# Kernel tuning notes

Hardware: AMD Instinct MI355X
Metric: run time of the kernel (lower is better)

Reference implementation:

```python
import jax, jax.numpy as jnp
import numpy as np

EPS = 1e-8
NUM_HEADS = 4


def setup_inputs() -> dict:
    key = jax.random.key(0)
    ks = jax.random.split(key, 20)
    N, D = 8192, 200      # total nodes, gnn/text dim
    B = 4                  # graphs (text batch)
    E, DEG = 4096, 16      # hyperedges, nodes per hyperedge
    H = 128                # fusion hidden dim
    f = lambda k, s: jax.random.normal(k, s, dtype=jnp.float32) * 0.05
    return {
        "x": jax.random.normal(ks[0], (N, D), dtype=jnp.float32),
        "text": jax.random.normal(ks[1], (B, D), dtype=jnp.float32),
        "W": f(ks[2], (D, D)),
        "b": jnp.zeros((D,), jnp.float32),
        "gate_w": f(ks[3], (D, 1)),
        "gate_b": jnp.zeros((1,), jnp.float32),
        "gnn_w": f(ks[4], (D, H)), "gnn_b": f(ks[5], (H,)),
        "text_w": f(ks[6], (D, H)), "text_b": f(ks[7], (H,)),
        "in_w": f(ks[8], (H, 3 * H)), "in_b": f(ks[9], (3 * H,)),
        "attn_out_w": f(ks[10], (H, H)), "attn_out_b": f(ks[11], (H,)),
        "fgate_w": f(ks[12], (2 * H, H)), "fgate_b": f(ks[13], (H,)),
        "outp_w": f(ks[14], (H, D)), "outp_b": f(ks[15], (D,)),
        "edge_nodes": jax.random.randint(ks[16], (E, DEG), 0, N),
    }


def _forward(x, text, W, b, gate_w, gate_b, gnn_w, gnn_b, text_w, text_b,
             in_w, in_b, attn_out_w, attn_out_b, fgate_w, fgate_b,
             outp_w, outp_b, edge_nodes):
    N, D = x.shape
    E, DEG = edge_nodes.shape
    # --- HypergraphConv: incidence build + normalized Laplacian propagation ---
    out = x @ W                                         # [N, D]
    # H[node, edge] = 1/len(edge); duplicates overwrite (set), as in torch loop
    Hinc = jnp.zeros((N, E), x.dtype).at[edge_nodes, jnp.arange(E)[:, None]].set(1.0 / DEG)
    Dv = Hinc.sum(axis=1)                               # node degree [N]
    De = Hinc.sum(axis=0)                               # edge degree [E]
    dv = 1.0 / jnp.sqrt(Dv + EPS)
    de = 1.0 / (De + EPS)
    Hl = Hinc * dv[:, None]                             # Dv^-1/2 H
    L = (Hl * de[None, :]) @ Hl.T                       # Dv^-1/2 H De^-1 H^T Dv^-1/2
    hyper_out = L @ out                                 # [N, D]
    alpha = jax.nn.sigmoid(x.mean(axis=0, keepdims=True) @ gate_w + gate_b)  # [1,1]
    gnn_feat = alpha * out + (1.0 - alpha) * hyper_out + b
    # --- CrossModalAttentionFusion on per-graph node features (3D path) ---
    B = text.shape[0]
    Nn = N // B
    gnn3 = gnn_feat.reshape(B, Nn, D)
    gp = gnn3 @ gnn_w + gnn_b                           # [B, Nn, H]
    tp = (text @ text_w + text_b)[:, None, :]           # [B, 1, H]
    Hd = gp.shape[-1]
    hd = Hd // NUM_HEADS
    q = gp @ in_w[:, :Hd] + in_b[:Hd]
    k = tp @ in_w[:, Hd:2 * Hd] + in_b[Hd:2 * Hd]
    v = tp @ in_w[:, 2 * Hd:] + in_b[2 * Hd:]
    qh = q.reshape(B, Nn, NUM_HEADS, hd).transpose(0, 2, 1, 3)   # [B,h,Nn,hd]
    kh = k.reshape(B, 1, NUM_HEADS, hd).transpose(0, 2, 1, 3)    # [B,h,1,hd]
    vh = v.reshape(B, 1, NUM_HEADS, hd).transpose(0, 2, 1, 3)
    scores = jnp.einsum("bhqd,bhkd->bhqk", qh, kh) / jnp.sqrt(jnp.float32(hd))
    attn = jax.nn.softmax(scores, axis=-1)              # kv_len=1 -> ones
    att = jnp.einsum("bhqk,bhkd->bhqd", attn, vh)
    att = att.transpose(0, 2, 1, 3).reshape(B, Nn, Hd) @ attn_out_w + attn_out_b
    g = jax.nn.sigmoid(jnp.concatenate([gp, att], axis=-1) @ fgate_w + fgate_b)
    fused = g * gp + (1.0 - g) * att
    return fused @ outp_w + outp_b                      # [B, Nn, D]


def reference(x, text, W, b, gate_w, gate_b, gnn_w, gnn_b, text_w, text_b,
              in_w, in_b, attn_out_w, attn_out_b, fgate_w, fgate_b,
              outp_w, outp_b, edge_nodes):
    return _forward(x, text, W, b, gate_w, gate_b, gnn_w, gnn_b, text_w, text_b,
                    in_w, in_b, attn_out_w, attn_out_b, fgate_w, fgate_b,
                    outp_w, outp_b, edge_nodes)
```

## Files before the change

kernel.cpp:

```cpp
#include <hip/hip_runtime.h>

#define NODES 8192
#define DIM   200
#define NEDGE 4096
#define DEGREE 16
#define HD    128
#define MT    16
#define ECAP  32
#define CPB   512

__device__ __forceinline__ float dv_of(int cnt) {
    return 1.0f / sqrtf((float)cnt * (1.0f / 16.0f) + 1e-8f);
}

__global__ void k_front(const float* __restrict__ W, const float* __restrict__ gnn_w,
                        const float* __restrict__ bias, const float* __restrict__ gnn_b,
                        const float* __restrict__ text, const float* __restrict__ text_w,
                        const float* __restrict__ text_b, const float* __restrict__ in_w,
                        const float* __restrict__ in_b, const float* __restrict__ aow,
                        const float* __restrict__ aob, const float* __restrict__ fgw,
                        const float* __restrict__ fgb, int* __restrict__ cnt,
                        float* __restrict__ Wg, float* __restrict__ bg,
                        float* __restrict__ attO, float* __restrict__ attg) {
    __shared__ float st[DIM];
    __shared__ float part[2][HD];
    __shared__ float vin[HD];
    int b = blockIdx.x, t = threadIdx.x;
    if (b < 32) {
        cnt[b * 256 + t] = 0;
        return;
    }
    if (b < 132) {
        int r = 2 * (b - 32) + (t >> 7);
        int c = t & 127;
        const float* vec = &W[r * DIM];
        float acc = 0.f;
        for (int k = 0; k < DIM; k++) acc += vec[k] * gnn_w[k * HD + c];
        Wg[r * HD + c] = acc;
        return;
    }
    if (b == 132) {
        if (t < HD) {
            float acc = 0.f;
            for (int k = 0; k < DIM; k++) acc += bias[k] * gnn_w[k * HD + t];
            bg[t] = acc + gnn_b[t];
        }
        return;
    }
    int g = b - 133;
    int c = t & 127, h = t >> 7;
    if (t < DIM) st[t] = text[g * DIM + t];
    __syncthreads();
    {
        float acc = 0.f;
        int k0 = h * 100;
        for (int k = k0; k < k0 + 100; k++) acc += st[k] * text_w[k * HD + c];
        part[h][c] = acc;
    }
    __syncthreads();
    if (t < HD) vin[t] = part[0][t] + part[1][t] + text_b[t];
    __syncthreads();
    {
        float acc = 0.f;
        int k0 = h * 64;
        for (int k = k0; k < k0 + 64; k++) acc += vin[k] * in_w[k * 3 * HD + 2 * HD + c];
        part[h][c] = acc;
    }
    __syncthreads();
    if (t < HD) vin[t] = part[0][t] + part[1][t] + in_b[2 * HD + t];
    __syncthreads();
    {
        float acc = 0.f;
        int k0 = h * 64;
        for (int k = k0; k < k0 + 64; k++) acc += vin[k] * aow[k * HD + c];
        part[h][c] = acc;
    }
    __syncthreads();
    if (t < HD) {
        float ao = part[0][t] + part[1][t] + aob[t];
        attO[g * HD + t] = ao;
        vin[t] = ao;
    }
    __syncthreads();
    {
        float acc = 0.f;
        int k0 = h * 64;
        for (int k = k0; k < k0 + 64; k++) acc += vin[k] * fgw[(HD + k) * HD + c];
        part[h][c] = acc;
    }
    __syncthreads();
    if (t < HD) attg[g * HD + t] = part[0][t] + part[1][t] + fgb[t];
}

__global__ void k_xwg(const float* __restrict__ x, const float* __restrict__ Wg,
                      const int* __restrict__ en, float* __restrict__ out2,
                      int* __restrict__ cnt, int* __restrict__ emask,
                      int* __restrict__ elist2, float* __restrict__ cpart) {
    __shared__ float sx[16 * DIM];
    int b = blockIdx.x, t = threadIdx.x;
    int bm = b * 16;
    const float4* x4 = (const float4*)(x + bm * DIM);
    float4* sx4 = (float4*)sx;
    for (int i = t; i < 16 * DIM / 4; i += 256) sx4[i] = x4[i];
    __syncthreads();
    if (t < DIM) {
        float s = 0.f;
#pragma unroll
        for (int r = 0; r < 16; r++) s += sx[r * DIM + t];
        cpart[b * DIM + t] = s;
    }
    int rg = t >> 6;
    int c0 = t & 63;
    float acc[4][2] = {{0.f,0.f},{0.f,0.f},{0.f,0.f},{0.f,0.f}};
    for (int k = 0; k < DIM; k++) {
        float w0 = Wg[k * HD + c0];
        float w1 = Wg[k * HD + c0 + 64];
#pragma unroll
        for (int i = 0; i < 4; i++) {
            float s = sx[(rg * 4 + i) * DIM + k];
            acc[i][0] += s * w0;
            acc[i][1] += s * w1;
        }
    }
#pragma unroll
    for (int i = 0; i < 4; i++) {
        out2[(bm + rg * 4 + i) * HD + c0]      = acc[i][0];
        out2[(bm + rg * 4 + i) * HD + c0 + 64] = acc[i][1];
    }
    if (t < 8) {
        int e = b * 8 + t;
        int idx[DEGREE];
#pragma unroll
        for (int i = 0; i < DEGREE; i++) idx[i] = en[e * DEGREE + i];
        int mask = 0;
#pragma unroll
        for (int i = 0; i < DEGREE; i++) {
            bool uniq = true;
            for (int j = 0; j < i; j++) uniq = uniq && (idx[j] != idx[i]);
            if (uniq) {
                mask |= (1 << i);
                int slot = atomicAdd(&cnt[idx[i]], 1);
                if (slot < ECAP) elist2[idx[i] * ECAP + slot] = e;
            }
        }
        emask[e] = mask;
    }
}

__global__ void k_tE(const int* __restrict__ en, const int* __restrict__ emask,
                     const int* __restrict__ cnt, const float* __restrict__ out2,
                     float* __restrict__ tE, const float* __restrict__ cpart,
                     const float* __restrict__ gate_w, const float* __restrict__ gate_b,
                     float* __restrict__ alpha) {
    int t = threadIdx.x;
    if (blockIdx.x == NEDGE / 2) {
        __shared__ float red[256];
        float v = 0.f;
        if (t < DIM) {
            float s = 0.f;
            for (int q = 0; q < CPB; q++) s += cpart[q * DIM + t];
            v = s * gate_w[t];
        }
        red[t] = v;
        __syncthreads();
        for (int o = 128; o > 0; o >>= 1) {
            if (t < o) red[t] += red[t + o];
            __syncthreads();
        }
        if (t == 0) {
            float z = red[0] / (float)NODES + gate_b[0];
            alpha[0] = 1.0f / (1.0f + expf(-z));
        }
        return;
    }
    int e = blockIdx.x * 2 + (t >> 7);
    int c = t & 127;
    int m = emask[e];
    float De = (float)__popc(m) * (1.0f / 16.0f);
    float de = 1.0f / (De + 1e-8f);
    int nd[DEGREE];
#pragma unroll
    for (int i = 0; i < DEGREE; i++) nd[i] = en[e * DEGREE + i];
    float acc = 0.f;
#pragma unroll
    for (int i = 0; i < DEGREE; i++)
        if ((m >> i) & 1) acc += dv_of(cnt[nd[i]]) * out2[nd[i] * HD + c];
    tE[e * HD + c] = de * acc;
}

__global__ void k_tail(const float* __restrict__ out2, const float* __restrict__ tE,
                       const int* __restrict__ cnt, const int* __restrict__ elist2,
                       const float* __restrict__ alpha, const float* __restrict__ bg,
                       const float* __restrict__ fgw, const float* __restrict__ attO,
                       const float* __restrict__ attg, const float* __restrict__ opw,
                       const float* __restrict__ opb, float* __restrict__ out) {
    __shared__ float sgp[MT][HD];
    __shared__ int   sid[MT][16];
    __shared__ int   scount[MT];
    int bm = blockIdx.x * MT;
    int gb = bm >> 11;
    int t = threadIdx.x;
    {
        int r = t >> 4, sl = t & 15;
        int n = bm + r;
        int cc = cnt[n]; cc = cc < ECAP ? cc : ECAP;
        if (sl == 0) scount[r] = cc;
        int ccs = cc < 16 ? cc : 16;
        sid[r][sl] = (sl < ccs) ? elist2[n * ECAP + sl] : 0;
    }
    __syncthreads();
    int c = t & 127, rg = t >> 7;
    float a = alpha[0];
    float bgc = bg[c];
#pragma unroll
    for (int i = 0; i < 8; i++) {
        int r = rg * 8 + i;
        int n = bm + r;
        int cc = scount[r];
        int ccs = cc < 16 ? cc : 16;
        float hyp = 0.f;
#pragma unroll
        for (int j = 0; j < 16; j++) {
            float v = tE[sid[r][j] * HD + c];
            hyp += (j < ccs) ? v : 0.f;
        }
        if (cc > 16)
            for (int j = 16; j < cc; j++) hyp += tE[elist2[n * ECAP + j] * HD + c];
        hyp *= dv_of(cnt[n]) * (1.0f / 256.0f);
        sgp[r][c] = a * out2[n * HD + c] + (1.0f - a) * hyp + bgc;
    }
    __syncthreads();
    float ao = attO[gb * HD + c];
    float ag = attg[gb * HD + c];
    float acc[8];
#pragma unroll
    for (int i = 0; i < 8; i++) acc[i] = ag;
    for (int j = 0; j < HD; j++) {
        float w = fgw[j * HD + c];
#pragma unroll
        for (int i = 0; i < 8; i++) acc[i] += sgp[rg * 8 + i][j] * w;
    }
    __syncthreads();
#pragma unroll
    for (int i = 0; i < 8; i++) {
        int r = rg * 8 + i;
        float g = 1.0f / (1.0f + expf(-acc[i]));
        sgp[r][c] = g * sgp[r][c] + (1.0f - g) * ao;
    }
    __syncthreads();
    if (t < DIM) {
        float accO[MT];
        float ob = opb[t];
#pragma unroll
        for (int i = 0; i < MT; i++) accO[i] = ob;
        for (int j = 0; j < HD; j++) {
            float w = opw[j * DIM + t];
#pragma unroll
            for (int i = 0; i < MT; i++) accO[i] += sgp[i][j] * w;
        }
#pragma unroll
        for (int i = 0; i < MT; i++) out[(bm + i) * DIM + t] = accO[i];
    }
}

extern "C" void kernel_launch(void* const* d_in, const int* in_sizes, int n_in,
                              void* d_out, int out_size, void* d_ws, size_t ws_size,
                              hipStream_t stream) {
    const float* x      = (const float*)d_in[0];
    const float* text   = (const float*)d_in[1];
    const float* W      = (const float*)d_in[2];
    const float* bias   = (const float*)d_in[3];
    const float* gate_w = (const float*)d_in[4];
    const float* gate_b = (const float*)d_in[5];
    const float* gnn_w  = (const float*)d_in[6];
    const float* gnn_b  = (const float*)d_in[7];
    const float* text_w = (const float*)d_in[8];
    const float* text_b = (const float*)d_in[9];
    const float* in_w   = (const float*)d_in[10];
    const float* in_b   = (const float*)d_in[11];
    const float* aow    = (const float*)d_in[12];
    const float* aob    = (const float*)d_in[13];
    const float* fgw    = (const float*)d_in[14];
    const float* fgb    = (const float*)d_in[15];
    const float* opw    = (const float*)d_in[16];
    const float* opb    = (const float*)d_in[17];
    const int*   en     = (const int*)d_in[18];
    float* out = (float*)d_out;

    char* q = (char*)d_ws;
    int*   cnt    = (int*)q;   q += NODES * sizeof(int);
    float* cpart  = (float*)q; q += (size_t)CPB * DIM * sizeof(float);
    float* out2   = (float*)q; q += (size_t)NODES * HD * sizeof(float);
    float* tE     = (float*)q; q += (size_t)NEDGE * HD * sizeof(float);
    int*   elist2 = (int*)q;   q += (size_t)NODES * ECAP * sizeof(int);
    float* Wg     = (float*)q; q += DIM * HD * sizeof(float);
    float* alpha  = (float*)q; q += sizeof(float);
    float* bg     = (float*)q; q += HD * sizeof(float);
    float* attO   = (float*)q; q += 4 * HD * sizeof(float);
    float* attg   = (float*)q; q += 4 * HD * sizeof(float);
    int*   emask  = (int*)q;   q += NEDGE * sizeof(int);

    k_front<<<137, 256, 0, stream>>>(W, gnn_w, bias, gnn_b, text, text_w, text_b,
                                     in_w, in_b, aow, aob, fgw, fgb,
                                     cnt, Wg, bg, attO, attg);
    k_xwg<<<512, 256, 0, stream>>>(x, Wg, en, out2, cnt, emask, elist2, cpart);
    k_tE<<<NEDGE / 2 + 1, 256, 0, stream>>>(en, emask, cnt, out2, tE,
                                            cpart, gate_w, gate_b, alpha);
    k_tail<<<NODES / MT, 256, 0, stream>>>(out2, tE, cnt, elist2, alpha, bg, fgw,
                                           attO, attg, opw, opb, out);
}
```

Measured before the change: 174.4 us.

## Halve tail tile rows, pad edge lists with a zero sentinel, trim front launch

The tail kernel now handles 8 nodes per block instead of 16, which doubles the block count and shrinks per-thread accumulators. Empty edge-list slots point at a new zero row of tE, so the gather needs no per-slot bounds test and reads up to 32 edges from shared memory. The count zeroing moves into the Wg-product blocks of the front kernel, which cuts that launch from 137 to 105 blocks. In k_xwg the dedup and atomic scatter now run before the GEMM, and the tE gather becomes a branchless select. The cost is an extra zero-row write, loads issued for masked-out nodes in tE, and more redundant reads of fgw and opw across the smaller tail blocks.

```diff
diff --git a/kernel.cpp b/kernel.cpp
--- a/kernel.cpp
+++ b/kernel.cpp
@@ -5,7 +5,7 @@
 #define NEDGE 4096
 #define DEGREE 16
 #define HD    128
-#define MT    16
+#define MT    8
 #define ECAP  32
 #define CPB   512
 
@@ -26,12 +26,9 @@
     __shared__ float part[2][HD];
     __shared__ float vin[HD];
     int b = blockIdx.x, t = threadIdx.x;
-    if (b < 32) {
-        cnt[b * 256 + t] = 0;
-        return;
-    }
-    if (b < 132) {
-        int r = 2 * (b - 32) + (t >> 7);
+    if (b < 100) {
+        if (b < 32) cnt[b * 256 + t] = 0;
+        int r = 2 * b + (t >> 7);
         int c = t & 127;
         const float* vec = &W[r * DIM];
         float acc = 0.f;
@@ -39,7 +36,7 @@
         Wg[r * HD + c] = acc;
         return;
     }
-    if (b == 132) {
+    if (b == 100) {
         if (t < HD) {
             float acc = 0.f;
             for (int k = 0; k < DIM; k++) acc += bias[k] * gnn_w[k * HD + t];
@@ -47,7 +44,7 @@
         }
         return;
     }
-    int g = b - 133;
+    int g = b - 101;
     int c = t & 127, h = t >> 7;
     if (t < DIM) st[t] = text[g * DIM + t];
     __syncthreads();
@@ -98,35 +95,6 @@
                       int* __restrict__ elist2, float* __restrict__ cpart) {
     __shared__ float sx[16 * DIM];
     int b = blockIdx.x, t = threadIdx.x;
-    int bm = b * 16;
-    const float4* x4 = (const float4*)(x + bm * DIM);
-    float4* sx4 = (float4*)sx;
-    for (int i = t; i < 16 * DIM / 4; i += 256) sx4[i] = x4[i];
-    __syncthreads();
-    if (t < DIM) {
-        float s = 0.f;
-#pragma unroll
-        for (int r = 0; r < 16; r++) s += sx[r * DIM + t];
-        cpart[b * DIM + t] = s;
-    }
-    int rg = t >> 6;
-    int c0 = t & 63;
-    float acc[4][2] = {{0.f,0.f},{0.f,0.f},{0.f,0.f},{0.f,0.f}};
-    for (int k = 0; k < DIM; k++) {
-        float w0 = Wg[k * HD + c0];
-        float w1 = Wg[k * HD + c0 + 64];
-#pragma unroll
-        for (int i = 0; i < 4; i++) {
-            float s = sx[(rg * 4 + i) * DIM + k];
-            acc[i][0] += s * w0;
-            acc[i][1] += s * w1;
-        }
-    }
-#pragma unroll
-    for (int i = 0; i < 4; i++) {
-        out2[(bm + rg * 4 + i) * HD + c0]      = acc[i][0];
-        out2[(bm + rg * 4 + i) * HD + c0 + 64] = acc[i][1];
-    }
     if (t < 8) {
         int e = b * 8 + t;
         int idx[DEGREE];
@@ -145,6 +113,35 @@
         }
         emask[e] = mask;
     }
+    int bm = b * 16;
+    const float4* x4 = (const float4*)(x + bm * DIM);
+    float4* sx4 = (float4*)sx;
+    for (int i = t; i < 16 * DIM / 4; i += 256) sx4[i] = x4[i];
+    __syncthreads();
+    if (t < DIM) {
+        float s = 0.f;
+#pragma unroll
+        for (int r = 0; r < 16; r++) s += sx[r * DIM + t];
+        cpart[b * DIM + t] = s;
+    }
+    int rg = t >> 6;
+    int c0 = t & 63;
+    float acc[4][2] = {{0.f,0.f},{0.f,0.f},{0.f,0.f},{0.f,0.f}};
+    for (int k = 0; k < DIM; k++) {
+        float w0 = Wg[k * HD + c0];
+        float w1 = Wg[k * HD + c0 + 64];
+#pragma unroll
+        for (int i = 0; i < 4; i++) {
+            float s = sx[(rg * 4 + i) * DIM + k];
+            acc[i][0] += s * w0;
+            acc[i][1] += s * w1;
+        }
+    }
+#pragma unroll
+    for (int i = 0; i < 4; i++) {
+        out2[(bm + rg * 4 + i) * HD + c0]      = acc[i][0];
+        out2[(bm + rg * 4 + i) * HD + c0 + 64] = acc[i][1];
+    }
 }
 
 __global__ void k_tE(const int* __restrict__ en, const int* __restrict__ emask,
@@ -154,6 +151,7 @@
                      float* __restrict__ alpha) {
     int t = threadIdx.x;
     if (blockIdx.x == NEDGE / 2) {
+        if (t < HD) tE[NEDGE * HD + t] = 0.f;
         __shared__ float red[256];
         float v = 0.f;
         if (t < DIM) {
@@ -183,8 +181,11 @@
     for (int i = 0; i < DEGREE; i++) nd[i] = en[e * DEGREE + i];
     float acc = 0.f;
 #pragma unroll
-    for (int i = 0; i < DEGREE; i++)
-        if ((m >> i) & 1) acc += dv_of(cnt[nd[i]]) * out2[nd[i] * HD + c];
+    for (int i = 0; i < DEGREE; i++) {
+        float dvv = dv_of(cnt[nd[i]]);
+        float vv  = out2[nd[i] * HD + c];
+        acc += ((m >> i) & 1) ? dvv * vv : 0.f;
+    }
     tE[e * HD + c] = de * acc;
 }
 
@@ -195,55 +196,47 @@
                        const float* __restrict__ attg, const float* __restrict__ opw,
                        const float* __restrict__ opb, float* __restrict__ out) {
     __shared__ float sgp[MT][HD];
-    __shared__ int   sid[MT][16];
+    __shared__ int   sid[MT][ECAP];
     __shared__ int   scount[MT];
     int bm = blockIdx.x * MT;
-    int gb = bm >> 11;
+    int b = bm >> 11;
     int t = threadIdx.x;
     {
-        int r = t >> 4, sl = t & 15;
+        int r = t >> 5, sl = t & 31;
         int n = bm + r;
         int cc = cnt[n]; cc = cc < ECAP ? cc : ECAP;
         if (sl == 0) scount[r] = cc;
-        int ccs = cc < 16 ? cc : 16;
-        sid[r][sl] = (sl < ccs) ? elist2[n * ECAP + sl] : 0;
+        sid[r][sl] = (sl < cc) ? elist2[n * ECAP + sl] : NEDGE;
     }
     __syncthreads();
     int c = t & 127, rg = t >> 7;
     float a = alpha[0];
     float bgc = bg[c];
 #pragma unroll
-    for (int i = 0; i < 8; i++) {
-        int r = rg * 8 + i;
+    for (int i = 0; i < 4; i++) {
+        int r = rg * 4 + i;
         int n = bm + r;
         int cc = scount[r];
-        int ccs = cc < 16 ? cc : 16;
         float hyp = 0.f;
 #pragma unroll
-        for (int j = 0; j < 16; j++) {
-            float v = tE[sid[r][j] * HD + c];
-            hyp += (j < ccs) ? v : 0.f;
-        }
-        if (cc > 16)
-            for (int j = 16; j < cc; j++) hyp += tE[elist2[n * ECAP + j] * HD + c];
+        for (int j = 0; j < 8; j++) hyp += tE[sid[r][j] * HD + c];
+        for (int j = 8; j < cc; j++) hyp += tE[sid[r][j] * HD + c];
         hyp *= dv_of(cnt[n]) * (1.0f / 256.0f);
         sgp[r][c] = a * out2[n * HD + c] + (1.0f - a) * hyp + bgc;
     }
     __syncthreads();
-    float ao = attO[gb * HD + c];
-    float ag = attg[gb * HD + c];
-    float acc[8];
-#pragma unroll
-    for (int i = 0; i < 8; i++) acc[i] = ag;
+    float ao = attO[b * HD + c];
+    float ag = attg[b * HD + c];
+    float acc[4] = {ag, ag, ag, ag};
     for (int j = 0; j < HD; j++) {
         float w = fgw[j * HD + c];
 #pragma unroll
-        for (int i = 0; i < 8; i++) acc[i] += sgp[rg * 8 + i][j] * w;
-    }
-    __syncthreads();
-#pragma unroll
-    for (int i = 0; i < 8; i++) {
-        int r = rg * 8 + i;
+        for (int i = 0; i < 4; i++) acc[i] += sgp[rg * 4 + i][j] * w;
+    }
+    __syncthreads();
+#pragma unroll
+    for (int i = 0; i < 4; i++) {
+        int r = rg * 4 + i;
         float g = 1.0f / (1.0f + expf(-acc[i]));
         sgp[r][c] = g * sgp[r][c] + (1.0f - g) * ao;
     }
@@ -291,7 +284,7 @@
     int*   cnt    = (int*)q;   q += NODES * sizeof(int);
     float* cpart  = (float*)q; q += (size_t)CPB * DIM * sizeof(float);
     float* out2   = (float*)q; q += (size_t)NODES * HD * sizeof(float);
-    float* tE     = (float*)q; q += (size_t)NEDGE * HD * sizeof(float);
+    float* tE     = (float*)q; q += (size_t)(NEDGE + 1) * HD * sizeof(float);
     int*   elist2 = (int*)q;   q += (size_t)NODES * ECAP * sizeof(int);
     float* Wg     = (float*)q; q += DIM * HD * sizeof(float);
     float* alpha  = (float*)q; q += sizeof(float);
@@ -300,7 +293,7 @@
     float* attg   = (float*)q; q += 4 * HD * sizeof(float);
     int*   emask  = (int*)q;   q += NEDGE * sizeof(int);
 
-    k_front<<<137, 256, 0, stream>>>(W, gnn_w, bias, gnn_b, text, text_w, text_b,
+    k_front<<<105, 256, 0, stream>>>(W, gnn_w, bias, gnn_b, text, text_w, text_b,
                                      in_w, in_b, aow, aob, fgw, fgb,
                                      cnt, Wg, bg, attO, attg);
     k_xwg<<<512, 256, 0, stream>>>(x, Wg, en, out2, cnt, emask, elist2, cpart);
```

New measurement: 165.3 us. 1.06x faster.
